# Optimization experiments

Hardware: AMD Instinct MI355X
Metric: run time of the kernel (lower is better)

The kernel has to match this reference:

```python
import jax, jax.numpy as jnp
import numpy as np

B, S, D = 2, 2048, 2048
H, HD = 16, 128
ROPE_THETA = 10000.0


def _rope_cos_sin(seq_len, head_dim, dtype=jnp.float32):
    inv_freq = 1.0 / (ROPE_THETA ** (jnp.arange(0, head_dim, 2, dtype=jnp.float32) / head_dim))
    t = jnp.arange(seq_len, dtype=jnp.float32)
    freqs = jnp.outer(t, inv_freq)                     # [S, HD/2]
    emb = jnp.concatenate([freqs, freqs], axis=-1)     # [S, HD]
    return jnp.cos(emb).astype(dtype), jnp.sin(emb).astype(dtype)


def _rotate_half(x):
    x1, x2 = jnp.split(x, 2, axis=-1)
    return jnp.concatenate([-x2, x1], axis=-1)


def _apply_rope(x, cos, sin):
    # x: [B, S, H, HD]; cos/sin: [S, HD] -> broadcast over batch and heads
    c = cos[None, :, None, :]
    s = sin[None, :, None, :]
    return x * c + _rotate_half(x) * s


def setup_inputs() -> dict:
    key = jax.random.key(0)
    ks = jax.random.split(key, 6)
    scale = 1.0 / np.sqrt(D)
    hidden_states = jax.random.normal(ks[0], (B, S, D), dtype=jnp.float32)
    # causal additive mask: 0 on/below diagonal, large negative above
    neg = jnp.finfo(jnp.float32).min
    causal = jnp.where(jnp.tril(jnp.ones((S, S), dtype=bool)), 0.0, neg)
    attention_mask = jnp.broadcast_to(causal[None, None, :, :], (B, 1, S, S)).astype(jnp.float32)
    Wq = jax.random.normal(ks[1], (D, D), dtype=jnp.float32) * scale
    Wk = jax.random.normal(ks[2], (D, D), dtype=jnp.float32) * scale
    Wv = jax.random.normal(ks[3], (D, D), dtype=jnp.float32) * scale
    Wo = jax.random.normal(ks[4], (D, D), dtype=jnp.float32) * scale
    return {"hidden_states": hidden_states, "attention_mask": attention_mask,
            "Wq": Wq, "Wk": Wk, "Wv": Wv, "Wo": Wo}


def reference(hidden_states, attention_mask, Wq, Wk, Wv, Wo):
    b, s, d = hidden_states.shape
    # projections (torch Linear: x @ W^T)
    q = (hidden_states @ Wq.T).reshape(b, s, H, HD)
    k = (hidden_states @ Wk.T).reshape(b, s, H, HD)
    v = (hidden_states @ Wv.T).reshape(b, s, H, HD)
    cos, sin = _rope_cos_sin(s, HD, hidden_states.dtype)
    q = _apply_rope(q, cos, sin)
    k = _apply_rope(k, cos, sin)
    # naive attention, [B, H, S, S] scores materialized as in the original
    scores = jnp.einsum('bqhd,bkhd->bhqk', q, k) / np.sqrt(HD)
    scores = scores + attention_mask
    attn = jax.nn.softmax(scores, axis=-1)
    out = jnp.einsum('bhqk,bkhd->bqhd', attn, v).reshape(b, s, d)
    return out @ Wo.T
```

## Files before the change

### kernel.cpp

```cpp
#include <hip/hip_runtime.h>
#include <hip/hip_bf16.h>

typedef __hip_bfloat16 bf16;
typedef __attribute__((ext_vector_type(8))) short s16x8;
typedef __attribute__((ext_vector_type(4))) float f32x4;
typedef __attribute__((ext_vector_type(16))) float f32x16;

#define MFMA16(a, b, c) __builtin_amdgcn_mfma_f32_16x16x32_bf16(a, b, c, 0, 0, 0)
#define MFMA32(a, b, c) __builtin_amdgcn_mfma_f32_32x32x16_bf16(a, b, c, 0, 0, 0)

#define GLL16(gsrc, ldst)                                                                 \
  __builtin_amdgcn_global_load_lds(                                                       \
      (const __attribute__((address_space(1))) unsigned int*)(gsrc),                      \
      (__attribute__((address_space(3))) unsigned int*)(ldst), 16, 0, 0)

#define VMCNT(n) asm volatile("s_waitcnt vmcnt(" #n ")" ::: "memory")
#define BARRIER() __builtin_amdgcn_s_barrier()

static constexpr int S_LEN = 2048;
static constexpr int D_DIM = 2048;
static constexpr int NY = 6144;

union BF4 { ushort4 u; bf16 b[4]; };

__device__ inline unsigned pack2(float a, float b) {
  union { bf16 h[2]; unsigned u; } x;
  x.h[0] = __float2bfloat16(a);
  x.h[1] = __float2bfloat16(b);
  return x.u;
}

__global__ void convert_all(const float* __restrict__ X, const float* __restrict__ Wq,
                            const float* __restrict__ Wk, const float* __restrict__ Wv,
                            const float* __restrict__ Wo, bf16* __restrict__ Xb,
                            bf16* __restrict__ Wb, bf16* __restrict__ Wob,
                            float* __restrict__ cosT, float* __restrict__ sinT) {
  int gid = blockIdx.x * 256 + threadIdx.x;
  if (gid < 6291456) {
    int i4 = gid * 4;
    const float* src;
    bf16* dst;
    int off;
    if (i4 < 8388608) {
      src = X; dst = Xb; off = i4;
    } else {
      int j = i4 - 8388608;
      int seg = j >> 22;
      off = j & 4194303;
      if (seg == 0) { src = Wq; dst = Wb; }
      else if (seg == 1) { src = Wk; dst = Wb + 4194304; }
      else if (seg == 2) { src = Wv; dst = Wb + 8388608; }
      else { src = Wo; dst = Wob; }
    }
    float4 v = *(const float4*)(src + off);
    BF4 o;
    o.b[0] = __float2bfloat16(v.x);
    o.b[1] = __float2bfloat16(v.y);
    o.b[2] = __float2bfloat16(v.z);
    o.b[3] = __float2bfloat16(v.w);
    *(ushort4*)(dst + off) = o.u;
  } else {
    int t4 = (gid - 6291456) * 4;
    if (t4 < 131072) {
#pragma unroll
      for (int k = 0; k < 4; ++k) {
        int i = t4 + k;
        int d = i & 63, s = i >> 6;
        float inv = powf(10000.0f, -(float)d * (1.0f / 64.0f));
        float ang = (float)s * inv;
        cosT[i] = cosf(ang);
        sinT[i] = sinf(ang);
      }
    }
  }
}

__device__ inline void storeC(float* p, float v) { *p = v; }
__device__ inline void storeC(bf16* p, float v) { *p = __float2bfloat16(v); }

__device__ __forceinline__ int permc(int c) {
  return (c & ~0x60) | ((c & 0x20) << 1) | ((c & 0x40) >> 1);
}

__global__ __launch_bounds__(512, 2) void gemm256_rope(const bf16* __restrict__ A,
                                                       const bf16* __restrict__ Bm,
                                                       bf16* __restrict__ C, int K, int lda,
                                                       int ldb, int ldc, int mt,
                                                       const float* __restrict__ cosT,
                                                       const float* __restrict__ sinT) {
  __shared__ __align__(16) char lds[131072];
  char* A0buf = lds;
  char* B0buf = lds + 32768;
  char* A1buf = lds + 65536;
  char* B1buf = lds + 98304;
  const int tid = threadIdx.x;
  const int lane = tid & 63;
  const int w = tid >> 6;
  const int wm = w >> 2, wn = w & 3;
  const int l15 = lane & 15, lh4 = lane >> 4;
  const int xr = l15 & 7;
  const int xo0 = ((lh4 ^ xr) << 4);
  const int xo1 = (((4 + lh4) ^ xr) << 4);

  const int nwg = gridDim.x;
  const int bid = blockIdx.x;
  const int swz = (bid & 7) * (nwg >> 3) + (bid >> 3);
  const int bm = swz % mt, bn = swz / mt;
  const int row0 = bm * 256, col0 = bn * 256;

  const int srow8 = lane >> 3;
  const int scol = ((lane & 7) ^ srow8) * 8;
  const bf16* gA_s = A + (size_t)(row0 + w * 8 + srow8) * lda + scol;
  const int hr0 = w * 8 + srow8;
  const int t0 = hr0 >> 5, lo5 = hr0 & 31;
  const bf16* gBp[2][2];
#pragma unroll
  for (int ch = 0; ch < 2; ++ch) {
#pragma unroll
    for (int r = 0; r < 2; ++r) {
      int c = (t0 + 2 * r) * 64 + ch * 32 + lo5;
      gBp[ch][r] = Bm + (size_t)(col0 + permc(c)) * ldb + scol;
    }
  }
  const int ldst = w * 1024;

#define STAGE_A(bufa, rh, k0)                                                     \
  {                                                                               \
    GLL16(gA_s + (size_t)((rh)*64) * lda + (k0), (bufa) + (rh)*16384 + ldst);     \
    GLL16(gA_s + (size_t)((rh)*64 + 128) * lda + (k0),                            \
          (bufa) + (rh)*16384 + 8192 + ldst);                                     \
  }
#define STAGE_B(bufb, ch, k0)                                                     \
  {                                                                               \
    GLL16(gBp[ch][0] + (k0), (bufb) + (ch)*16384 + ldst);                         \
    GLL16(gBp[ch][1] + (k0), (bufb) + (ch)*16384 + 8192 + ldst);                  \
  }

  f32x4 acc[8][4];
#pragma unroll
  for (int i = 0; i < 8; ++i)
#pragma unroll
    for (int j = 0; j < 4; ++j) acc[i][j] = (f32x4){0.f, 0.f, 0.f, 0.f};

  s16x8 af[4][2];
  s16x8 bfr[2][2];

#define READ_AH(bufa, rh)                                                         \
  _Pragma("unroll") for (int ii = 0; ii < 4; ++ii) {                              \
    const char* p_ = (bufa) + (rh)*16384 + (wm * 64 + ii * 16 + l15) * 128;       \
    af[ii][0] = *(const s16x8*)(p_ + xo0);                                        \
    af[ii][1] = *(const s16x8*)(p_ + xo1);                                        \
  }
#define READ_BH(bufb, ch)                                                         \
  _Pragma("unroll") for (int jj = 0; jj < 2; ++jj) {                              \
    const char* p_ = (bufb) + (ch)*16384 + (wn * 32 + jj * 16 + l15) * 128;       \
    bfr[jj][0] = *(const s16x8*)(p_ + xo0);                                       \
    bfr[jj][1] = *(const s16x8*)(p_ + xo1);                                       \
  }
#define QUAD(rh, ch)                                                              \
  __builtin_amdgcn_s_setprio(1);                                                  \
  _Pragma("unroll") for (int jj = 0; jj < 2; ++jj)                                \
  _Pragma("unroll") for (int ii = 0; ii < 4; ++ii)                                \
  _Pragma("unroll") for (int ks = 0; ks < 2; ++ks)                                \
      acc[(rh)*4 + ii][(ch)*2 + jj] =                                             \
          MFMA16(af[ii][ks], bfr[jj][ks], acc[(rh)*4 + ii][(ch)*2 + jj]);         \
  __builtin_amdgcn_s_setprio(0);

  STAGE_A(A0buf, 0, 0);
  STAGE_B(B0buf, 0, 0);
  STAGE_B(B0buf, 1, 0);
  STAGE_A(A0buf, 1, 0);
  STAGE_A(A1buf, 0, 64);
  STAGE_B(B1buf, 1, 64);
  STAGE_A(A1buf, 1, 64);
  VMCNT(6);
  BARRIER();

  const int NI = K >> 7;
  for (int i = 0; i < NI; ++i) {
    const int kT1 = (2 * i + 1) << 6;
    const int kT2 = (2 * i + 2) << 6;
    const int kT3 = (2 * i + 3) << 6;
    const bool nl = (i + 1 < NI);
    READ_AH(A0buf, 0);
    READ_BH(B0buf, 0);
    STAGE_B(B1buf, 0, kT1);
    BARRIER();
    QUAD(0, 0);
    BARRIER();
    READ_BH(B0buf, 1);
    if (nl) STAGE_A(A0buf, 0, kT2);
    BARRIER();
    QUAD(0, 1);
    BARRIER();
    READ_AH(A0buf, 1);
    if (nl) STAGE_B(B0buf, 1, kT2);
    BARRIER();
    QUAD(1, 1);
    BARRIER();
    READ_BH(B0buf, 0);
    if (nl) STAGE_A(A0buf, 1, kT2);
    BARRIER();
    QUAD(1, 0);
    if (nl) { VMCNT(6); } else { VMCNT(0); }
    BARRIER();
    READ_AH(A1buf, 0);
    READ_BH(B1buf, 0);
    if (nl) STAGE_B(B0buf, 0, kT2);
    BARRIER();
    QUAD(0, 0);
    BARRIER();
    READ_BH(B1buf, 1);
    if (nl) STAGE_A(A1buf, 0, kT3);
    BARRIER();
    QUAD(0, 1);
    BARRIER();
    READ_AH(A1buf, 1);
    if (nl) STAGE_B(B1buf, 1, kT3);
    BARRIER();
    QUAD(1, 1);
    BARRIER();
    READ_BH(B1buf, 0);
    if (nl) STAGE_A(A1buf, 1, kT3);
    BARRIER();
    QUAD(1, 0);
    if (nl) { VMCNT(6); }
    BARRIER();
  }
#undef STAGE_A
#undef STAGE_B
#undef READ_AH
#undef READ_BH
#undef QUAD

  const float qsc = (col0 < 2048) ? 0.12751682f : 1.0f;
  const int dbase = (wn & 1) * 32 + l15;
  const int gcbase = col0 + (wn >> 1) * 128 + (wn & 1) * 32 + l15;
#pragma unroll
  for (int ri = 0; ri < 8; ++ri) {
    const int s0r = row0 + wm * 128 + ri * 16 + lh4 * 4;
#pragma unroll
    for (int pp = 0; pp < 2; ++pp) {
      const int d = dbase + pp * 16;
      const int gclo = gcbase + pp * 16;
#pragma unroll
      for (int rr = 0; rr < 4; ++rr) {
        const int srow = (s0r + rr) & (S_LEN - 1);
        float cs = cosT[srow * 64 + d];
        float sn = sinT[srow * 64 + d];
        float lo = acc[ri][pp][rr], hi = acc[ri][pp + 2][rr];
        C[(size_t)(s0r + rr) * ldc + gclo] = __float2bfloat16((lo * cs - hi * sn) * qsc);
        C[(size_t)(s0r + rr) * ldc + gclo + 64] = __float2bfloat16((hi * cs + lo * sn) * qsc);
      }
    }
  }
}

template <typename OutT, bool TRANSV>
__global__ __launch_bounds__(512, 2) void gemm_fine(const bf16* __restrict__ A,
                                                    const bf16* __restrict__ Bm,
                                                    OutT* __restrict__ C, int K, int lda,
                                                    int ldb, int ldc, int mt) {
  __shared__ __align__(16) char lds[147456];
  char* b0 = lds;
  char* b1 = lds + 49152;
  char* b2 = lds + 98304;
  const int tid = threadIdx.x;
  const int lane = tid & 63;
  const int w = tid >> 6;
  const int wm = w >> 2, wn = w & 3;
  const int l15 = lane & 15, lh4 = lane >> 4;
  const int xr = l15 & 7;
  const int xo0 = ((lh4 ^ xr) << 4);
  const int xo1 = (((4 + lh4) ^ xr) << 4);

  const int nwg = gridDim.x;
  const int bid = blockIdx.x;
  const int swz = (bid & 7) * (nwg >> 3) + (bid >> 3);
  const int bm = swz % mt, bn = swz / mt;
  const int row0 = bm * 128, col0 = bn * 256;

  const int srow = w * 8 + (lane >> 3);
  const int scol = ((lane & 7) ^ (lane >> 3)) * 8;
  const bf16* gA = A + (size_t)(row0 + srow) * lda + scol;
  const bf16* gB = Bm + (size_t)(col0 + srow) * ldb + scol;
  const int ldst = w * 1024;

  f32x4 acc[4][4];
#pragma unroll
  for (int i = 0; i < 4; ++i)
#pragma unroll
    for (int j = 0; j < 4; ++j) acc[i][j] = (f32x4){0.f, 0.f, 0.f, 0.f};

  s16x8 af[4], bfr[4];

#define PH_READ(BUF, XO)                                                          \
  _Pragma("unroll") for (int ii = 0; ii < 4; ++ii)                                \
      af[ii] = *(const s16x8*)((BUF) + (wm * 64 + ii * 16 + l15) * 128 + (XO));   \
  _Pragma("unroll") for (int jj = 0; jj < 4; ++jj)                                \
      bfr[jj] = *(const s16x8*)((BUF) + 16384 + (wn * 64 + jj * 16 + l15) * 128 + (XO));
#define PH_FMA()                                                                  \
  __builtin_amdgcn_s_setprio(1);                                                  \
  _Pragma("unroll") for (int jj = 0; jj < 4; ++jj)                                \
  _Pragma("unroll") for (int ii = 0; ii < 4; ++ii)                                \
      acc[ii][jj] = MFMA16(af[ii], bfr[jj], acc[ii][jj]);                         \
  __builtin_amdgcn_s_setprio(0);
#define STAGE_T(BUF, kS)                                                          \
  GLL16(gA + (kS), (BUF) + ldst);                                                 \
  GLL16(gA + (size_t)64 * lda + (kS), (BUF) + 8192 + ldst);                       \
  GLL16(gB + (kS), (BUF) + 16384 + ldst);                                         \
  GLL16(gB + (size_t)64 * ldb + (kS), (BUF) + 24576 + ldst);                      \
  GLL16(gB + (size_t)128 * ldb + (kS), (BUF) + 32768 + ldst);                     \
  GLL16(gB + (size_t)192 * ldb + (kS), (BUF) + 40960 + ldst);
#define TILE_MAIN(RBUF, SBUF, kS)                                                 \
  PH_READ(RBUF, xo0);                                                             \
  GLL16(gA + (kS), (SBUF) + ldst);                                                \
  GLL16(gA + (size_t)64 * lda + (kS), (SBUF) + 8192 + ldst);                      \
  GLL16(gB + (kS), (SBUF) + 16384 + ldst);                                        \
  BARRIER();                                                                      \
  PH_FMA();                                                                       \
  BARRIER();                                                                      \
  PH_READ(RBUF, xo1);                                                             \
  GLL16(gB + (size_t)64 * ldb + (kS), (SBUF) + 24576 + ldst);                     \
  GLL16(gB + (size_t)128 * ldb + (kS), (SBUF) + 32768 + ldst);                    \
  GLL16(gB + (size_t)192 * ldb + (kS), (SBUF) + 40960 + ldst);                    \
  BARRIER();                                                                      \
  PH_FMA();                                                                       \
  VMCNT(6);                                                                       \
  BARRIER();

  STAGE_T(b0, 0);
  STAGE_T(b1, 64);
  VMCNT(6);
  BARRIER();

  const int NT = K >> 6;
  for (int t = 0; t < NT - 2; t += 3) {
    TILE_MAIN(b0, b2, (size_t)(t + 2) * 64);
    TILE_MAIN(b1, b0, (size_t)(t + 3) * 64);
    TILE_MAIN(b2, b1, (size_t)(t + 4) * 64);
  }
  PH_READ(b0, xo0);
  BARRIER();
  PH_FMA();
  BARRIER();
  PH_READ(b0, xo1);
  BARRIER();
  PH_FMA();
  VMCNT(0);
  BARRIER();
  PH_READ(b1, xo0);
  BARRIER();
  PH_FMA();
  BARRIER();
  PH_READ(b1, xo1);
  BARRIER();
  PH_FMA();
#undef PH_READ
#undef PH_FMA
#undef STAGE_T
#undef TILE_MAIN

  if constexpr (TRANSV) {
    bf16* Vt = (bf16*)C;
#pragma unroll
    for (int mi = 0; mi < 4; ++mi)
#pragma unroll
      for (int ni = 0; ni < 4; ++ni) {
        int gr = row0 + wm * 64 + mi * 16 + lh4 * 4;
        int gc = col0 + wn * 64 + ni * 16 + l15;
        size_t vrow = (size_t)((gr >> 11) * 2048 + gc);
        BF4 o;
#pragma unroll
        for (int rr = 0; rr < 4; ++rr) o.b[rr] = __float2bfloat16(acc[mi][ni][rr]);
        *(ushort4*)(Vt + vrow * S_LEN + (gr & (S_LEN - 1))) = o.u;
      }
  } else {
#pragma unroll
    for (int mi = 0; mi < 4; ++mi)
#pragma unroll
      for (int ni = 0; ni < 4; ++ni) {
        int gr = row0 + wm * 64 + mi * 16 + lh4 * 4;
        int gc = col0 + wn * 64 + ni * 16 + l15;
#pragma unroll
        for (int rr = 0; rr < 4; ++rr)
          storeC(&C[(size_t)(gr + rr) * ldc + gc], acc[mi][ni][rr]);
      }
  }
}

__global__ __launch_bounds__(256, 2) void attn_fwd(const bf16* __restrict__ Y,
                                                   const bf16* __restrict__ Vt,
                                                   bf16* __restrict__ At) {
  __shared__ __align__(16) char smem[65536];

  const int idx = blockIdx.x;
  const int qt = (idx < 256) ? (15 - (idx >> 5)) : ((idx - 256) >> 5);
  const int bh = idx & 31;
  const int b = bh >> 4, h = bh & 15;
  const int tid = threadIdx.x;
  const int lane = tid & 63;
  const int w = tid >> 6;
  const int l31 = lane & 31;
  const int hi = lane >> 5;
  const int q0w = qt * 128 + w * 32;
  const int q = q0w + l31;

  s16x8 qf[8];
  {
    const bf16* qb = Y + (size_t)(b * S_LEN + q) * NY + h * 128 + hi * 8;
#pragma unroll
    for (int s = 0; s < 8; ++s) qf[s] = *(const s16x8*)(qb + s * 16);
  }

  f32x16 O[4];
#pragma unroll
  for (int d = 0; d < 4; ++d)
#pragma unroll
    for (int e = 0; e < 16; ++e) O[d][e] = 0.f;
  float m_run = -3.0e38f, l_run = 0.f;

  const bf16* Kbase = Y + (size_t)(b * S_LEN) * NY + 2048 + h * 128;
  const bf16* Vbase = Vt + (size_t)bh * 128 * S_LEN;
  const int tmax = 2 * qt + 1;

  const int rk_ = w * 4 + (lane >> 4);
  const int ck_ = lane & 15;
  const int dv_ = w * 8 + (lane >> 3);
  const int cv_ = lane & 7;

#define STAGE_KV(T, BASE)                                                         \
  {                                                                               \
    const int kv0s = (T)*64;                                                      \
    _Pragma("unroll") for (int j = 0; j < 4; ++j) {                               \
      int rk = j * 16 + rk_;                                                      \
      GLL16(Kbase + (size_t)(kv0s + rk) * NY + ((ck_ ^ (rk & 15)) * 8),           \
            (BASE) + (j * 4096 + w * 1024));                                      \
      int dv = j * 32 + dv_;                                                      \
      GLL16(Vbase + (size_t)dv * S_LEN + kv0s + ((cv_ ^ (dv & 7)) * 8),           \
            (BASE) + 16384 + (j * 4096 + w * 1024));                              \
    }                                                                             \
  }

  STAGE_KV(0, smem);

  for (int t = 0; t <= tmax; ++t) {
    const int kv0 = t * 64;
    const char* cur = smem + (t & 1) * 32768;
    BARRIER();
    if (t < tmax) {
      STAGE_KV(t + 1, smem + ((t + 1) & 1) * 32768);
      VMCNT(8);
    } else {
      VMCNT(0);
    }
    BARRIER();
    if (kv0 > q0w + 31) continue;

    float sv[32];
#pragma unroll
    for (int tt = 0; tt < 2; ++tt) {
      f32x16 se, so;
#pragma unroll
      for (int e = 0; e < 16; ++e) { se[e] = 0.f; so[e] = 0.f; }
      const int rk = tt * 32 + l31;
      const char* kr = cur + rk * 256;
      const int xr = (rk & 15) << 4;
      __builtin_amdgcn_s_setprio(1);
#pragma unroll
      for (int s = 0; s < 8; s += 2) {
        s16x8 kf0 = *(const s16x8*)(kr + ((s * 32 + hi * 16) ^ xr));
        se = MFMA32(kf0, qf[s], se);
        s16x8 kf1 = *(const s16x8*)(kr + (((s + 1) * 32 + hi * 16) ^ xr));
        so = MFMA32(kf1, qf[s + 1], so);
      }
      __builtin_amdgcn_s_setprio(0);
#pragma unroll
      for (int e = 0; e < 16; ++e) sv[tt * 16 + e] = se[e] + so[e];
    }

    if (kv0 + 63 > q0w) {
#pragma unroll
      for (int tt = 0; tt < 2; ++tt)
#pragma unroll
        for (int r = 0; r < 16; ++r) {
          int kvr = kv0 + tt * 32 + (r & 3) + 8 * (r >> 2) + 4 * hi;
          if (kvr > q) sv[tt * 16 + r] = -3.0e38f;
        }
    }

    float m8[8];
#pragma unroll
    for (int i = 0; i < 8; ++i)
      m8[i] = fmaxf(fmaxf(sv[i], sv[i + 8]), fmaxf(sv[i + 16], sv[i + 24]));
    float m2a = fmaxf(fmaxf(m8[0], m8[1]), fmaxf(m8[2], m8[3]));
    float m2b = fmaxf(fmaxf(m8[4], m8[5]), fmaxf(m8[6], m8[7]));
    float pmax = fmaxf(fmaxf(m2a, m2b), __shfl_xor(fmaxf(m2a, m2b), 32, 64));

    bool need = pmax > m_run + 11.54f;
    if (__any(need)) {
      float newm = fmaxf(m_run, pmax);
      float ef = exp2f(m_run - newm);
      m_run = newm;
      l_run *= ef;
#pragma unroll
      for (int d = 0; d < 4; ++d)
#pragma unroll
        for (int e = 0; e < 16; ++e) O[d][e] *= ef;
    }

#pragma unroll
    for (int i = 0; i < 32; ++i) sv[i] = exp2f(sv[i] - m_run);
    float s16v[16];
#pragma unroll
    for (int i = 0; i < 16; ++i) s16v[i] = sv[i] + sv[i + 16];
    float s8v[8];
#pragma unroll
    for (int i = 0; i < 8; ++i) s8v[i] = s16v[i] + s16v[i + 8];
    float s4v[4];
#pragma unroll
    for (int i = 0; i < 4; ++i) s4v[i] = s8v[i] + s8v[i + 4];
    float rsum = (s4v[0] + s4v[1]) + (s4v[2] + s4v[3]);
    rsum += __shfl_xor(rsum, 32, 64);
    l_run += rsum;

    unsigned pw[4][4];
#pragma unroll
    for (int tt = 0; tt < 2; ++tt) {
      const int bs = tt * 16;
      unsigned x01 = pack2(sv[bs + 0], sv[bs + 1]);
      unsigned x23 = pack2(sv[bs + 2], sv[bs + 3]);
      unsigned x45 = pack2(sv[bs + 4], sv[bs + 5]);
      unsigned x67 = pack2(sv[bs + 6], sv[bs + 7]);
      unsigned y01 = pack2(sv[bs + 8], sv[bs + 9]);
      unsigned y23 = pack2(sv[bs + 10], sv[bs + 11]);
      unsigned y45 = pack2(sv[bs + 12], sv[bs + 13]);
      unsigned y67 = pack2(sv[bs + 14], sv[bs + 15]);
      asm volatile("v_permlane32_swap_b32 %0, %1" : "+v"(x01), "+v"(x45));
      asm volatile("v_permlane32_swap_b32 %0, %1" : "+v"(x23), "+v"(x67));
      asm volatile("v_permlane32_swap_b32 %0, %1" : "+v"(y01), "+v"(y45));
      asm volatile("v_permlane32_swap_b32 %0, %1" : "+v"(y23), "+v"(y67));
      pw[tt * 2][0] = x01;
      pw[tt * 2][1] = x23;
      pw[tt * 2][2] = x45;
      pw[tt * 2][3] = x67;
      pw[tt * 2 + 1][0] = y01;
      pw[tt * 2 + 1][1] = y23;
      pw[tt * 2 + 1][2] = y45;
      pw[tt * 2 + 1][3] = y67;
    }

#pragma unroll
    for (int dt = 0; dt < 4; ++dt) {
      const int d = dt * 32 + l31;
      const char* vr = cur + 16384 + d * 128;
      const int xv = (d & 7) << 4;
      __builtin_amdgcn_s_setprio(1);
#pragma unroll
      for (int sl = 0; sl < 4; ++sl) {
        s16x8 vf = *(const s16x8*)(vr + ((sl * 32 + hi * 16) ^ xv));
        union { unsigned u[4]; s16x8 v; } pb;
        pb.u[0] = pw[sl][0];
        pb.u[1] = pw[sl][1];
        pb.u[2] = pw[sl][2];
        pb.u[3] = pw[sl][3];
        O[dt] = MFMA32(vf, pb.v, O[dt]);
      }
      __builtin_amdgcn_s_setprio(0);
    }
  }
#undef STAGE_KV

  __syncthreads();
  const float inv = 1.0f / l_run;
  {
    const int orow = w * 32 + l31;
    const int xo = (orow & 15) << 4;
    char* obase = (char*)smem + orow * 256;
#pragma unroll
    for (int dt = 0; dt < 4; ++dt)
#pragma unroll
      for (int r = 0; r < 16; ++r) {
        int d = dt * 32 + (r & 3) + 8 * (r >> 2) + 4 * hi;
        *(bf16*)(obase + ((d * 2) ^ xo)) = __float2bfloat16(O[dt][r] * inv);
      }
  }
  __syncthreads();
  bf16* dst = At + (size_t)(b * S_LEN + qt * 128) * D_DIM + h * 128;
#pragma unroll
  for (int j = 0; j < 8; ++j) {
    int id = j * 256 + tid;
    int rr = id >> 4, cc = id & 15;
    int4 val = *(const int4*)((char*)smem + rr * 256 + ((cc * 16) ^ ((rr & 15) << 4)));
    *(int4*)(dst + (size_t)rr * D_DIM + cc * 8) = val;
  }
}

extern "C" void kernel_launch(void* const* d_in, const int* in_sizes, int n_in,
                              void* d_out, int out_size, void* d_ws, size_t ws_size,
                              hipStream_t stream) {
  const float* X = (const float*)d_in[0];
  const float* Wq = (const float*)d_in[2];
  const float* Wk = (const float*)d_in[3];
  const float* Wv = (const float*)d_in[4];
  const float* Wo = (const float*)d_in[5];
  float* out = (float*)d_out;
  char* ws = (char*)d_ws;

  bf16* Xb = (bf16*)(ws);
  bf16* Wb = (bf16*)(ws + 16777216);
  bf16* Wob = (bf16*)(ws + 41943040);
  bf16* Y = (bf16*)(ws + 50331648);
  bf16* Vt = (bf16*)(ws + 100663296);
  bf16* At = (bf16*)(ws + 117440512);
  float* cosT = (float*)(ws + 134217728);
  float* sinT = (float*)(ws + 134742016);

  convert_all<<<24704, 256, 0, stream>>>(X, Wq, Wk, Wv, Wo, Xb, Wb, Wob, cosT, sinT);

  gemm256_rope<<<256, 512, 0, stream>>>(Xb, Wb, Y, 2048, 2048, 2048, 6144, 16, cosT, sinT);
  gemm_fine<bf16, true><<<256, 512, 0, stream>>>(Xb, Wb + (size_t)4096 * 2048, Vt,
                                                 2048, 2048, 2048, 2048, 32);
  attn_fwd<<<512, 256, 0, stream>>>(Y, Vt, At);
  gemm_fine<float, false><<<256, 512, 0, stream>>>(At, Wob, out, 2048, 2048, 2048, 2048, 32);
}
```

Baseline: 237.4 us.

## Split KV range for long causal query tiles and merge partials in combine kernel

Query tiles 8-15, which have the longest causal KV ranges, are each split into two blocks that process halves of the KV tiles and write unnormalized fp32 partial outputs plus running max and sum. A new combine kernel merges each pair using log-sum-exp weights and writes the bf16 attention output. Short tiles still run unsplit. This evens out per-block work and raises the block count to cut tail imbalance, at the cost of an extra launch and fp32 partial traffic through workspace that reuses the input-conversion buffers.

```diff
diff --git a/kernel.cpp b/kernel.cpp
--- a/kernel.cpp
+++ b/kernel.cpp
@@ -391,11 +391,28 @@
 
 __global__ __launch_bounds__(256, 2) void attn_fwd(const bf16* __restrict__ Y,
                                                    const bf16* __restrict__ Vt,
-                                                   bf16* __restrict__ At) {
+                                                   bf16* __restrict__ At,
+                                                   float* __restrict__ Opart,
+                                                   float* __restrict__ Ml) {
   __shared__ __align__(16) char smem[65536];
 
   const int idx = blockIdx.x;
-  const int qt = (idx < 256) ? (15 - (idx >> 5)) : ((idx - 256) >> 5);
+  int qt, tA, tB, sid;
+  bool split;
+  if (idx < 512) {
+    split = true;
+    qt = 15 - (idx >> 6);
+    const int half = (idx >> 5) & 1;
+    tA = half ? (qt + 1) : 0;
+    tB = half ? (2 * qt + 1) : qt;
+    sid = ((qt - 8) << 6) | (half << 5) | (idx & 31);
+  } else {
+    split = false;
+    qt = 7 - ((idx - 512) >> 5);
+    tA = 0;
+    tB = 2 * qt + 1;
+    sid = 0;
+  }
   const int bh = idx & 31;
   const int b = bh >> 4, h = bh & 15;
   const int tid = threadIdx.x;
@@ -422,7 +439,6 @@
 
   const bf16* Kbase = Y + (size_t)(b * S_LEN) * NY + 2048 + h * 128;
   const bf16* Vbase = Vt + (size_t)bh * 128 * S_LEN;
-  const int tmax = 2 * qt + 1;
 
   const int rk_ = w * 4 + (lane >> 4);
   const int ck_ = lane & 15;
@@ -442,13 +458,13 @@
     }                                                                             \
   }
 
-  STAGE_KV(0, smem);
-
-  for (int t = 0; t <= tmax; ++t) {
+  STAGE_KV(tA, smem + (tA & 1) * 32768);
+
+  for (int t = tA; t <= tB; ++t) {
     const int kv0 = t * 64;
     const char* cur = smem + (t & 1) * 32768;
     BARRIER();
-    if (t < tmax) {
+    if (t < tB) {
       STAGE_KV(t + 1, smem + ((t + 1) & 1) * 32768);
       VMCNT(8);
     } else {
@@ -571,28 +587,82 @@
   }
 #undef STAGE_KV
 
-  __syncthreads();
-  const float inv = 1.0f / l_run;
-  {
-    const int orow = w * 32 + l31;
-    const int xo = (orow & 15) << 4;
-    char* obase = (char*)smem + orow * 256;
+  if (split) {
+    const int qlocal = w * 32 + l31;
+    float* op = Opart + (size_t)sid * 16384 + qlocal * 128;
 #pragma unroll
     for (int dt = 0; dt < 4; ++dt)
 #pragma unroll
-      for (int r = 0; r < 16; ++r) {
-        int d = dt * 32 + (r & 3) + 8 * (r >> 2) + 4 * hi;
-        *(bf16*)(obase + ((d * 2) ^ xo)) = __float2bfloat16(O[dt][r] * inv);
+      for (int rq = 0; rq < 4; ++rq) {
+        int d0 = dt * 32 + 8 * rq + 4 * hi;
+        f32x4 v;
+        v[0] = O[dt][rq * 4 + 0];
+        v[1] = O[dt][rq * 4 + 1];
+        v[2] = O[dt][rq * 4 + 2];
+        v[3] = O[dt][rq * 4 + 3];
+        *(f32x4*)(op + d0) = v;
       }
-  }
-  __syncthreads();
-  bf16* dst = At + (size_t)(b * S_LEN + qt * 128) * D_DIM + h * 128;
-#pragma unroll
-  for (int j = 0; j < 8; ++j) {
-    int id = j * 256 + tid;
-    int rr = id >> 4, cc = id & 15;
-    int4 val = *(const int4*)((char*)smem + rr * 256 + ((cc * 16) ^ ((rr & 15) << 4)));
-    *(int4*)(dst + (size_t)rr * D_DIM + cc * 8) = val;
+    if (hi == 0) {
+      Ml[sid * 256 + qlocal] = m_run;
+      Ml[sid * 256 + 128 + qlocal] = l_run;
+    }
+  } else {
+    __syncthreads();
+    const float inv = 1.0f / l_run;
+    {
+      const int orow = w * 32 + l31;
+      const int xo = (orow & 15) << 4;
+      char* obase = (char*)smem + orow * 256;
+#pragma unroll
+      for (int dt = 0; dt < 4; ++dt)
+#pragma unroll
+        for (int r = 0; r < 16; ++r) {
+          int d = dt * 32 + (r & 3) + 8 * (r >> 2) + 4 * hi;
+          *(bf16*)(obase + ((d * 2) ^ xo)) = __float2bfloat16(O[dt][r] * inv);
+        }
+    }
+    __syncthreads();
+    bf16* dst = At + (size_t)(b * S_LEN + qt * 128) * D_DIM + h * 128;
+#pragma unroll
+    for (int j = 0; j < 8; ++j) {
+      int id = j * 256 + tid;
+      int rr = id >> 4, cc = id & 15;
+      int4 val = *(const int4*)((char*)smem + rr * 256 + ((cc * 16) ^ ((rr & 15) << 4)));
+      *(int4*)(dst + (size_t)rr * D_DIM + cc * 8) = val;
+    }
+  }
+}
+
+__global__ __launch_bounds__(256) void attn_combine(const float* __restrict__ Opart,
+                                                    const float* __restrict__ Ml,
+                                                    bf16* __restrict__ At) {
+  const int cid = blockIdx.x;
+  const int qt = 8 + (cid >> 5);
+  const int bh = cid & 31;
+  const int b = bh >> 4, h = bh & 15;
+  const int s0 = ((qt - 8) << 6) | bh;
+  const int s1 = s0 | 32;
+  const int t = threadIdx.x;
+  const int row = t >> 1;
+  const int dseg = (t & 1) * 64;
+  float m0 = Ml[s0 * 256 + row], l0 = Ml[s0 * 256 + 128 + row];
+  float m1 = Ml[s1 * 256 + row], l1 = Ml[s1 * 256 + 128 + row];
+  float m = fmaxf(m0, m1);
+  float w0 = exp2f(m0 - m), w1 = exp2f(m1 - m);
+  float inv = 1.0f / (w0 * l0 + w1 * l1);
+  const float* p0 = Opart + (size_t)s0 * 16384 + row * 128 + dseg;
+  const float* p1 = Opart + (size_t)s1 * 16384 + row * 128 + dseg;
+  bf16* dst = At + (size_t)(b * S_LEN + qt * 128 + row) * D_DIM + h * 128 + dseg;
+#pragma unroll
+  for (int j = 0; j < 16; ++j) {
+    float4 a = *(const float4*)(p0 + j * 4);
+    float4 c = *(const float4*)(p1 + j * 4);
+    BF4 o;
+    o.b[0] = __float2bfloat16((w0 * a.x + w1 * c.x) * inv);
+    o.b[1] = __float2bfloat16((w0 * a.y + w1 * c.y) * inv);
+    o.b[2] = __float2bfloat16((w0 * a.z + w1 * c.z) * inv);
+    o.b[3] = __float2bfloat16((w0 * a.w + w1 * c.w) * inv);
+    *(ushort4*)(dst + j * 4) = o.u;
   }
 }
 
@@ -615,12 +685,15 @@
   bf16* At = (bf16*)(ws + 117440512);
   float* cosT = (float*)(ws + 134217728);
   float* sinT = (float*)(ws + 134742016);
+  float* Opart = (float*)(ws);
+  float* Ml = (float*)(ws + 33554432);
 
   convert_all<<<24704, 256, 0, stream>>>(X, Wq, Wk, Wv, Wo, Xb, Wb, Wob, cosT, sinT);
 
   gemm256_rope<<<256, 512, 0, stream>>>(Xb, Wb, Y, 2048, 2048, 2048, 6144, 16, cosT, sinT);
   gemm_fine<bf16, true><<<256, 512, 0, stream>>>(Xb, Wb + (size_t)4096 * 2048, Vt,
                                                  2048, 2048, 2048, 2048, 32);
-  attn_fwd<<<512, 256, 0, stream>>>(Y, Vt, At);
+  attn_fwd<<<768, 256, 0, stream>>>(Y, Vt, At, Opart, Ml);
+  attn_combine<<<256, 256, 0, stream>>>(Opart, Ml, At);
   gemm_fine<float, false><<<256, 512, 0, stream>>>(At, Wob, out, 2048, 2048, 2048, 2048, 32);
 }
```

Measured after the change: 259.0 us. 9.1% more time.
